# Kernel tuning notes

Hardware: AMD Instinct MI355X
Metric: run time of the kernel (lower is better)

## Reference

```python
import jax, jax.numpy as jnp
import numpy as np

N = 20000; E = 320000; IN = 128; H = 6; C = 64; HC = H * C; NC = 16; NG = 64


def _gatv2(x, src, dst, wl, bl, wr, br, att, bias, heads, out_c, concat):
    # PyG GATv2Conv (eval mode, share_weights=False, negative_slope=0.2)
    n = x.shape[0]
    xl = (x @ wl + bl).reshape(n, heads, out_c)   # source-side transform
    xr = (x @ wr + br).reshape(n, heads, out_c)   # target-side transform
    # edge-wise attention logits: leaky_relu(x_l[j] + x_r[i]) . att
    e = jnp.einsum('ehc,hc->eh', jax.nn.leaky_relu(xl[src] + xr[dst], 0.2), att)
    # segment softmax over incoming edges of each target node
    emax = jax.ops.segment_max(e, dst, num_segments=n)
    a = jnp.exp(e - emax[dst])
    denom = jax.ops.segment_sum(a, dst, num_segments=n)
    alpha = a / (denom[dst] + 1e-16)
    out = jax.ops.segment_sum(xl[src] * alpha[:, :, None], dst, num_segments=n)
    out = out.reshape(n, heads * out_c) if concat else out.mean(axis=1)
    return out + bias


def setup_inputs() -> dict:
    key = jax.random.key(0)
    ks = jax.random.split(key, 32)
    s = 0.05
    inp = {}
    inp['x'] = jax.random.normal(ks[0], (N, IN), jnp.float32)
    inp['edge_index'] = jax.random.randint(ks[1], (2, E), 0, N, dtype=jnp.int32)
    inp['batch'] = jnp.sort(jax.random.randint(ks[2], (N,), 0, NG, dtype=jnp.int32))
    # input projection (input_dim != hidden_dim * n_heads)
    inp['inp_w'] = jax.random.normal(ks[3], (IN, HC), jnp.float32) * s
    inp['inp_b'] = jnp.zeros((HC,), jnp.float32)
    # layer 0: IN -> (H, C), concat
    inp['l0_wl'] = jax.random.normal(ks[4], (IN, HC), jnp.float32) * s
    inp['l0_bl'] = jnp.zeros((HC,), jnp.float32)
    inp['l0_wr'] = jax.random.normal(ks[5], (IN, HC), jnp.float32) * s
    inp['l0_br'] = jnp.zeros((HC,), jnp.float32)
    inp['l0_att'] = jax.random.normal(ks[6], (H, C), jnp.float32) * s
    inp['l0_bias'] = jnp.zeros((HC,), jnp.float32)
    # layer 1: HC -> (H, C), concat
    inp['l1_wl'] = jax.random.normal(ks[7], (HC, HC), jnp.float32) * s
    inp['l1_bl'] = jnp.zeros((HC,), jnp.float32)
    inp['l1_wr'] = jax.random.normal(ks[8], (HC, HC), jnp.float32) * s
    inp['l1_br'] = jnp.zeros((HC,), jnp.float32)
    inp['l1_att'] = jax.random.normal(ks[9], (H, C), jnp.float32) * s
    inp['l1_bias'] = jnp.zeros((HC,), jnp.float32)
    # layer 2: HC -> (1, C), no concat (mean over the single head)
    inp['l2_wl'] = jax.random.normal(ks[10], (HC, C), jnp.float32) * s
    inp['l2_bl'] = jnp.zeros((C,), jnp.float32)
    inp['l2_wr'] = jax.random.normal(ks[11], (HC, C), jnp.float32) * s
    inp['l2_br'] = jnp.zeros((C,), jnp.float32)
    inp['l2_att'] = jax.random.normal(ks[12], (1, C), jnp.float32) * s
    inp['l2_bias'] = jnp.zeros((C,), jnp.float32)
    # residual projection HC -> C at the last layer (bias-free Linear)
    inp['res_w'] = jax.random.normal(ks[13], (HC, C), jnp.float32) * s
    # dense head: Linear(C,C) + BatchNorm1d(eval) + ReLU + Linear(C,NC)
    inp['d1_w'] = jax.random.normal(ks[14], (C, C), jnp.float32) * s
    inp['d1_b'] = jnp.zeros((C,), jnp.float32)
    inp['bn_g'] = jnp.ones((C,), jnp.float32)
    inp['bn_b'] = jnp.zeros((C,), jnp.float32)
    inp['bn_m'] = jnp.zeros((C,), jnp.float32)
    inp['bn_v'] = jnp.ones((C,), jnp.float32)
    inp['d2_w'] = jax.random.normal(ks[15], (C, NC), jnp.float32) * s
    inp['d2_b'] = jnp.zeros((NC,), jnp.float32)
    return inp


def reference(x, edge_index, batch, inp_w, inp_b,
              l0_wl, l0_bl, l0_wr, l0_br, l0_att, l0_bias,
              l1_wl, l1_bl, l1_wr, l1_br, l1_att, l1_bias,
              l2_wl, l2_bl, l2_wr, l2_br, l2_att, l2_bias,
              res_w, d1_w, d1_b, bn_g, bn_b, bn_m, bn_v, d2_w, d2_b):
    n = x.shape[0]
    sl = jnp.arange(n, dtype=edge_index.dtype)           # self-loops (PyG default)
    src = jnp.concatenate([edge_index[0], sl])
    dst = jnp.concatenate([edge_index[1], sl])
    x_res = x @ inp_w + inp_b
    h = jax.nn.elu(_gatv2(x, src, dst, l0_wl, l0_bl, l0_wr, l0_br, l0_att, l0_bias, H, C, True)) + x_res
    x_res = h
    h = jax.nn.elu(_gatv2(h, src, dst, l1_wl, l1_bl, l1_wr, l1_br, l1_att, l1_bias, H, C, True)) + x_res
    x_res = h
    h = jax.nn.elu(_gatv2(h, src, dst, l2_wl, l2_bl, l2_wr, l2_br, l2_att, l2_bias, 1, C, False)) + x_res @ res_w
    pooled = jax.ops.segment_sum(h, batch, num_segments=NG)
    z = pooled @ d1_w + d1_b
    z = (z - bn_m) / jnp.sqrt(bn_v + 1e-5) * bn_g + bn_b  # BatchNorm1d eval
    z = jax.nn.relu(z) @ d2_w + d2_b
    return h, z
```

## Files before the change

kernel.cpp:

```cpp
#include <hip/hip_runtime.h>
#include <hip/hip_bf16.h>
#include <math.h>

#define NN 20000
#define EE 320000
#define IND 128
#define HH 6
#define CC 64
#define HCC 384
#define NCC 16
#define NGG 64

typedef __bf16 bf16x8 __attribute__((ext_vector_type(8)));
typedef float f32x4 __attribute__((ext_vector_type(4)));
typedef float f32x2 __attribute__((ext_vector_type(2)));
typedef unsigned short ushort_t;
typedef unsigned int uint_t;

#define LOG2E 1.44269504088896f

__device__ inline ushort_t f2bf(float f) {
    union { float f; uint_t u; } x; x.f = f;
    uint_t r = (x.u + 0x7FFF + ((x.u >> 16) & 1)) >> 16;
    return (ushort_t)r;
}
__device__ inline void bf8cvt2(uint4 v, f32x2* f) {
    union { uint_t u; float x; } a, b;
    a.u = v.x << 16; b.u = v.x & 0xFFFF0000u; f[0] = (f32x2){a.x, b.x};
    a.u = v.y << 16; b.u = v.y & 0xFFFF0000u; f[1] = (f32x2){a.x, b.x};
    a.u = v.z << 16; b.u = v.z & 0xFFFF0000u; f[2] = (f32x2){a.x, b.x};
    a.u = v.w << 16; b.u = v.w & 0xFFFF0000u; f[3] = (f32x2){a.x, b.x};
}

template <int CTRL>
__device__ inline float dppadd(float x) {
    int y = __builtin_amdgcn_mov_dpp(__builtin_bit_cast(int, x), CTRL, 0xF, 0xF, true);
    return x + __builtin_bit_cast(float, y);
}

__device__ inline void load_lds16(const ushort_t* g, ushort_t* l) {
    __builtin_amdgcn_global_load_lds(
        (const __attribute__((address_space(1))) void*)g,
        (__attribute__((address_space(3))) void*)l, 16, 0, 0);
}


__global__ void zero_init_kernel(int* counts, int* s6_tail, int* s1_tail, int n) {
    int t = blockIdx.x * blockDim.x + threadIdx.x;
    if (t < n) counts[t] = 0;
    if (t < 8) { s6_tail[t] = 0; s1_tail[t] = 0; }
}

__global__ void count_kernel(const int* __restrict__ ei, int* __restrict__ counts, int E) {
    int t = blockIdx.x * blockDim.x + threadIdx.x;
    if (t < E) atomicAdd(&counts[ei[E + t]], 1);
}

__global__ __launch_bounds__(1024) void scan_kernel(
    const int* __restrict__ counts, int* __restrict__ offsets,
    int* __restrict__ cursor, int n) {
    __shared__ int buf[NN];
    __shared__ int part[1024];
    int t = threadIdx.x;
    for (int idx = t; idx < n; idx += 1024) buf[idx] = counts[idx] + 1;
    __syncthreads();
    int per = (n + 1023) / 1024;
    int base = t * per;
    int sum = 0;
    for (int j = 0; j < per; ++j) {
        int idx = base + j;
        if (idx < n) sum += buf[idx];
    }
    part[t] = sum;
    __syncthreads();
    for (int off = 1; off < 1024; off <<= 1) {
        int v = (t >= off) ? part[t - off] : 0;
        __syncthreads();
        part[t] += v;
        __syncthreads();
    }
    int run = (t == 0) ? 0 : part[t - 1];
    for (int j = 0; j < per; ++j) {
        int idx = base + j;
        if (idx < n) {
            int deg = buf[idx];
            buf[idx] = run;
            run += deg;
        }
    }
    __syncthreads();
    for (int idx = t; idx < n; idx += 1024) {
        int v = buf[idx];
        offsets[idx] = v;
        cursor[idx] = v;
    }
    if (t == 1023) offsets[n] = run;
}

__global__ void fill_kernel(const int* __restrict__ ei, int* __restrict__ cursor,
                            int* __restrict__ srcs6, int* __restrict__ srcs1,
                            int E, int n) {
    int t = blockIdx.x * blockDim.x + threadIdx.x;
    if (t < E) {
        int s = ei[t];
        int d = ei[E + t];
        int slot = atomicAdd(&cursor[d], 1);
        srcs6[slot] = s * 1536;
        srcs1[slot] = s << 8;
    } else if (t < E + n) {
        int i = t - E;
        int slot = atomicAdd(&cursor[i], 1);
        srcs6[slot] = i * 1536;
        srcs1[slot] = i << 8;
    }
}

#define WBIG (1152 * IND)
#define WC1 (768 * HCC)
#define WC2 (192 * HCC)
#define XB_N (NN * IND)
#define PREP_TOTAL (WBIG + WC1 + WC2 + XB_N + 1152 + 768 + 192)

__global__ void prep_kernel(const float* __restrict__ x, const float* __restrict__ inp_w,
    const float* __restrict__ l0wl, const float* __restrict__ l0wr,
    const float* __restrict__ l1wl, const float* __restrict__ l1wr,
    const float* __restrict__ l2wl, const float* __restrict__ l2wr,
    const float* __restrict__ resw,
    const float* __restrict__ inp_b,
    const float* __restrict__ l0bl, const float* __restrict__ l0br,
    const float* __restrict__ l1bl, const float* __restrict__ l1br,
    const float* __restrict__ l2bl, const float* __restrict__ l2br,
    ushort_t* wBig, ushort_t* wC1, ushort_t* wC2, ushort_t* xb,
    float* bBig, float* bC1, float* bC2)
{
    int i = blockIdx.x * blockDim.x + threadIdx.x;
    if (i >= PREP_TOTAL) return;
    if (i < WBIG) {
        int col = i >> 7, k = i & 127;
        float v;
        if (col < 384)      v = inp_w[k * 384 + col];
        else if (col < 768) v = l0wl[k * 384 + (col - 384)];
        else                v = l0wr[k * 384 + (col - 768)];
        wBig[i] = f2bf(v); return;
    }
    i -= WBIG;
    if (i < WC1) {
        int col = i / 384, k = i - col * 384;
        float v = col < 384 ? l1wl[k * 384 + col] : l1wr[k * 384 + (col - 384)];
        wC1[i] = f2bf(v); return;
    }
    i -= WC1;
    if (i < WC2) {
        int col = i / 384, k = i - col * 384;
        float v;
        if (col < 64)       v = resw[k * 64 + col];
        else if (col < 128) v = l2wl[k * 64 + (col - 64)];
        else                v = l2wr[k * 64 + (col - 128)];
        wC2[i] = f2bf(v); return;
    }
    i -= WC2;
    if (i < XB_N) { xb[i] = f2bf(x[i]); return; }
    i -= XB_N;
    if (i < 1152) {
        float v;
        if (i < 384)      v = inp_b[i];
        else if (i < 768) v = l0bl[i - 384];
        else              v = l0br[i - 768];
        bBig[i] = v; return;
    }
    i -= 1152;
    if (i < 768) { bC1[i] = i < 384 ? l1bl[i] : l1br[i - 384]; return; }
    i -= 768;
    if (i < 192) {
        float v;
        if (i < 64)       v = 0.0f;
        else if (i < 128) v = l2bl[i - 64];
        else              v = l2br[i - 128];
        bC2[i] = v; return;
    }
}

__global__ __launch_bounds__(512) void gemm_mfma2(
    const ushort_t* __restrict__ A, const ushort_t* __restrict__ BT,
    const float* __restrict__ bias,
    ushort_t* __restrict__ Cb1, int ld1,
    ushort_t* __restrict__ Cb2, int ld2, int split,
    int M, int N, int K, int NT)
{
    __shared__ ushort_t Bs[2][2][128 * 32];
    int t = threadIdx.x;
    int w = t >> 6, L = t & 63;
    int m0 = blockIdx.x * 256;
    int q = L >> 4, r16 = L & 15;
    int lr = L >> 2;
    int lc = ((L & 3) ^ ((lr >> 1) & 3)) * 8;
    int sw = (q ^ ((r16 >> 1) & 3)) * 8;
    int oB = (w * 16) * 32;

    int rA0 = min(m0 + w * 32 + r16, M - 1);
    int rA1 = min(m0 + w * 32 + 16 + r16, M - 1);
    const ushort_t* pA0base = A + (size_t)rA0 * K + q * 8;
    const ushort_t* pA1base = A + (size_t)rA1 * K + q * 8;

    for (int nt = 0; nt < NT; ++nt) {
        int n0 = (blockIdx.y * NT + nt) * 128;
        int rB = min(n0 + w * 16 + lr, N - 1);
        const ushort_t* gB = BT + (size_t)rB * K + lc;
        const ushort_t* pA0 = pA0base;
        const ushort_t* pA1 = pA1base;

        f32x4 acc[2][8];
#pragma unroll
        for (int a = 0; a < 2; ++a)
#pragma unroll
            for (int b = 0; b < 8; ++b) acc[a][b] = (f32x4){0.f, 0.f, 0.f, 0.f};

        load_lds16(gB, &Bs[0][0][oB]);
        load_lds16(gB + 32, &Bs[0][1][oB]);
        gB += 64;
        bf16x8 a0 = *(const bf16x8*)pA0;
        bf16x8 a2 = *(const bf16x8*)(pA0 + 32);
        bf16x8 a1 = *(const bf16x8*)pA1;
        bf16x8 a3 = *(const bf16x8*)(pA1 + 32);
        pA0 += 64; pA1 += 64;

        int buf = 0;
        for (int k0 = 0; k0 < K; k0 += 64) {
            __syncthreads();
            bool more = (k0 + 64 < K);
            if (more) {
                int nb = buf ^ 1;
                load_lds16(gB, &Bs[nb][0][oB]);
                load_lds16(gB + 32, &Bs[nb][1][oB]);
                gB += 64;
            }
            bf16x8 na0, na1, na2, na3;
            if (more) {
                na0 = *(const bf16x8*)pA0;
                na2 = *(const bf16x8*)(pA0 + 32);
                na1 = *(const bf16x8*)pA1;
                na3 = *(const bf16x8*)(pA1 + 32);
                pA0 += 64; pA1 += 64;
            }
#pragma unroll
            for (int ct = 0; ct < 8; ++ct) {
                bf16x8 blo = *(const bf16x8*)&Bs[buf][0][(ct * 16 + r16) * 32 + sw];
                bf16x8 bhi = *(const bf16x8*)&Bs[buf][1][(ct * 16 + r16) * 32 + sw];
                acc[0][ct] = __builtin_amdgcn_mfma_f32_16x16x32_bf16(blo, a0, acc[0][ct], 0, 0, 0);
                acc[1][ct] = __builtin_amdgcn_mfma_f32_16x16x32_bf16(blo, a1, acc[1][ct], 0, 0, 0);
                acc[0][ct] = __builtin_amdgcn_mfma_f32_16x16x32_bf16(bhi, a2, acc[0][ct], 0, 0, 0);
                acc[1][ct] = __builtin_amdgcn_mfma_f32_16x16x32_bf16(bhi, a3, acc[1][ct], 0, 0, 0);
            }
            if (more) { a0 = na0; a1 = na1; a2 = na2; a3 = na3; }
            buf ^= 1;
        }
#pragma unroll
        for (int rt = 0; rt < 2; ++rt) {
            int row = m0 + w * 32 + rt * 16 + r16;
            if (row >= M) continue;
#pragma unroll
            for (int ct = 0; ct < 8; ++ct) {
                int colb = n0 + ct * 16 + q * 4;
                if (colb >= N) continue;
                float4 bv = *(const float4*)(bias + colb);
                uint2 pk;
                pk.x = (uint_t)f2bf(acc[rt][ct][0] + bv.x) | ((uint_t)f2bf(acc[rt][ct][1] + bv.y) << 16);
                pk.y = (uint_t)f2bf(acc[rt][ct][2] + bv.z) | ((uint_t)f2bf(acc[rt][ct][3] + bv.w) << 16);
                if (colb < split)
                    *(uint2*)(Cb1 + (size_t)row * ld1 + colb) = pk;
                else
                    *(uint2*)(Cb2 + (size_t)row * ld2 + (colb - split)) = pk;
            }
        }
    }
}

__global__ __launch_bounds__(256) void gemm_mfma(
    const ushort_t* __restrict__ A, const ushort_t* __restrict__ BT,
    const float* __restrict__ bias,
    float* __restrict__ Cf, ushort_t* __restrict__ Cb1, int ld1,
    ushort_t* __restrict__ Cb2, int ld2, int split,
    int M, int N, int K)
{
    __shared__ ushort_t Bs[2][2][128 * 32];
    int t = threadIdx.x;
    int w = t >> 6, L = t & 63;
    int m0 = blockIdx.x * 128, n0 = blockIdx.y * 128;
    int q = L >> 4, r16 = L & 15;

    f32x4 acc[2][8];
#pragma unroll
    for (int a = 0; a < 2; ++a)
#pragma unroll
        for (int b = 0; b < 8; ++b) acc[a][b] = (f32x4){0.f, 0.f, 0.f, 0.f};

    int lr = L >> 2;
    int lc = ((L & 3) ^ ((lr >> 1) & 3)) * 8;
    int rB0 = min(n0 + w * 32 + lr, N - 1);
    int rB1 = min(n0 + w * 32 + 16 + lr, N - 1);
    const ushort_t* gB0 = BT + (size_t)rB0 * K + lc;
    const ushort_t* gB1 = BT + (size_t)rB1 * K + lc;
    int oB0 = (w * 32) * 32;
    int oB1 = (w * 32 + 16) * 32;

    int rA0 = min(m0 + w * 32 + r16, M - 1);
    int rA1 = min(m0 + w * 32 + 16 + r16, M - 1);
    const ushort_t* pA0 = A + (size_t)rA0 * K + q * 8;
    const ushort_t* pA1 = A + (size_t)rA1 * K + q * 8;

    int sw = (q ^ ((r16 >> 1) & 3)) * 8;

    load_lds16(gB0, &Bs[0][0][oB0]);
    load_lds16(gB1, &Bs[0][0][oB1]);
    load_lds16(gB0 + 32, &Bs[0][1][oB0]);
    load_lds16(gB1 + 32, &Bs[0][1][oB1]);
    gB0 += 64; gB1 += 64;
    bf16x8 a0 = *(const bf16x8*)pA0;
    bf16x8 a2 = *(const bf16x8*)(pA0 + 32);
    bf16x8 a1 = *(const bf16x8*)pA1;
    bf16x8 a3 = *(const bf16x8*)(pA1 + 32);
    pA0 += 64; pA1 += 64;

    int buf = 0;
    for (int k0 = 0; k0 < K; k0 += 64) {
        __syncthreads();
        bool more = (k0 + 64 < K);
        if (more) {
            int nb = buf ^ 1;
            load_lds16(gB0, &Bs[nb][0][oB0]);
            load_lds16(gB1, &Bs[nb][0][oB1]);
            load_lds16(gB0 + 32, &Bs[nb][1][oB0]);
            load_lds16(gB1 + 32, &Bs[nb][1][oB1]);
            gB0 += 64; gB1 += 64;
        }
        bf16x8 na0, na1, na2, na3;
        if (more) {
            na0 = *(const bf16x8*)pA0;
            na2 = *(const bf16x8*)(pA0 + 32);
            na1 = *(const bf16x8*)pA1;
            na3 = *(const bf16x8*)(pA1 + 32);
            pA0 += 64; pA1 += 64;
        }
#pragma unroll
        for (int ct = 0; ct < 8; ++ct) {
            bf16x8 blo = *(const bf16x8*)&Bs[buf][0][(ct * 16 + r16) * 32 + sw];
            bf16x8 bhi = *(const bf16x8*)&Bs[buf][1][(ct * 16 + r16) * 32 + sw];
            acc[0][ct] = __builtin_amdgcn_mfma_f32_16x16x32_bf16(blo, a0, acc[0][ct], 0, 0, 0);
            acc[1][ct] = __builtin_amdgcn_mfma_f32_16x16x32_bf16(blo, a1, acc[1][ct], 0, 0, 0);
            acc[0][ct] = __builtin_amdgcn_mfma_f32_16x16x32_bf16(bhi, a2, acc[0][ct], 0, 0, 0);
            acc[1][ct] = __builtin_amdgcn_mfma_f32_16x16x32_bf16(bhi, a3, acc[1][ct], 0, 0, 0);
        }
        if (more) { a0 = na0; a1 = na1; a2 = na2; a3 = na3; }
        buf ^= 1;
    }
#pragma unroll
    for (int rt = 0; rt < 2; ++rt) {
        int row = m0 + w * 32 + rt * 16 + r16;
        if (row >= M) continue;
#pragma unroll
        for (int ct = 0; ct < 8; ++ct) {
            int colb = n0 + ct * 16 + q * 4;
            if (colb >= N) continue;
            float4 bv = *(const float4*)(bias + colb);
            float v0 = acc[rt][ct][0] + bv.x;
            float v1 = acc[rt][ct][1] + bv.y;
            float v2 = acc[rt][ct][2] + bv.z;
            float v3 = acc[rt][ct][3] + bv.w;
            if (colb < split) {
                if (Cf) {
                    *(float4*)(Cf + (size_t)row * ld1 + colb) = make_float4(v0, v1, v2, v3);
                } else {
                    uint2 pk;
                    pk.x = (uint_t)f2bf(v0) | ((uint_t)f2bf(v1) << 16);
                    pk.y = (uint_t)f2bf(v2) | ((uint_t)f2bf(v3) << 16);
                    *(uint2*)(Cb1 + (size_t)row * ld1 + colb) = pk;
                }
            } else {
                uint2 pk;
                pk.x = (uint_t)f2bf(v0) | ((uint_t)f2bf(v1) << 16);
                pk.y = (uint_t)f2bf(v2) | ((uint_t)f2bf(v3) << 16);
                *(uint2*)(Cb2 + (size_t)row * ld2 + (colb - split)) = pk;
            }
        }
    }
}

__global__ __launch_bounds__(128) void gat6_kernel(
    const ushort_t* __restrict__ cat, const float* __restrict__ att,
    const float* __restrict__ bias, const ushort_t* __restrict__ resB,
    ushort_t* __restrict__ outB,
    const int* __restrict__ offsets, const int* __restrict__ srcs6, int n)
{
    int wid = (blockIdx.x * blockDim.x + threadIdx.x) >> 6;
    if (wid >= n) return;
    int lane = threadIdx.x & 63;
    int h = lane >> 3, c8 = lane & 7;
    bool hv = h < HH;
    int off = h * 64 + c8 * 8;
    int offL2 = (hv ? off : off - 384) * 2;
    int i = wid;
    int beg = __builtin_amdgcn_readfirstlane(offsets[i]);
    int end = __builtin_amdgcn_readfirstlane(offsets[i + 1]);
    int deg = end - beg;
    int P = (deg + 1) >> 1;
    const char* catc = (const char*)cat;

    f32x2 xr2[4], att2[4];
    {
        uint4 v = *(const uint4*)(catc + (size_t)i * 1536 + 768 + offL2);
        bf8cvt2(v, xr2);
    }
#pragma unroll
    for (int j = 0; j < 4; ++j) {
        int o = (offL2 >> 1) + 2 * j;
        att2[j] = (f32x2){att[o] * LOG2E, att[o + 1] * LOG2E};
    }

    float s = 0.0f;
    f32x2 acc2[4];
#pragma unroll
    for (int j = 0; j < 4; ++j) acc2[j] = (f32x2){0.f, 0.f};

    int bA0 = srcs6[beg], bB0 = srcs6[beg + 1];
    uint4 cA = *(const uint4*)(catc + (size_t)(uint_t)bA0 + offL2);
    uint4 cB = *(const uint4*)(catc + (size_t)(uint_t)bB0 + offL2);
    int iA1 = srcs6[beg + 2], iB1 = srcs6[beg + 3];

    for (int p = 0; p < P; ++p) {
        uint4 nA = cA, nB = cB;
        bool pre = (p + 1 < P);
        if (pre) {
            nA = *(const uint4*)(catc + (size_t)(uint_t)iA1 + offL2);
            nB = *(const uint4*)(catc + (size_t)(uint_t)iB1 + offL2);
            iA1 = srcs6[beg + 2 * p + 4];
            iB1 = srcs6[beg + 2 * p + 5];
        }
        f32x2 xlA[4], xlB[4];
        bf8cvt2(cA, xlA);
        bf8cvt2(cB, xlB);
        f32x2 pA2 = (f32x2){0.f, 0.f}, pB2 = (f32x2){0.f, 0.f};
#pragma unroll
        for (int j = 0; j < 4; ++j) {
            f32x2 ta = xlA[j] + xr2[j];
            ta = __builtin_elementwise_max(ta, ta * 0.2f);
            pA2 += ta * att2[j];
            f32x2 tb = xlB[j] + xr2[j];
            tb = __builtin_elementwise_max(tb, tb * 0.2f);
            pB2 += tb * att2[j];
        }
        float pA = pA2.x + pA2.y, pB = pB2.x + pB2.y;
        pA = dppadd<0xB1>(pA);
        pB = dppadd<0xB1>(pB);
        pA = dppadd<0x4E>(pA);
        pB = dppadd<0x4E>(pB);
        pA = dppadd<0x141>(pA);
        pB = dppadd<0x141>(pB);
        float wA = __builtin_amdgcn_exp2f(pA);
        float wB = (2 * p + 1 < deg) ? __builtin_amdgcn_exp2f(pB) : 0.0f;
        s += wA + wB;
        f32x2 wA2 = (f32x2){wA, wA}, wB2 = (f32x2){wB, wB};
#pragma unroll
        for (int j = 0; j < 4; ++j) {
            acc2[j] += wA2 * xlA[j];
            acc2[j] += wB2 * xlB[j];
        }
        cA = nA; cB = nB;
    }

    if (hv) {
        float inv = 1.0f / (s + 1e-16f);
        size_t ob = (size_t)i * HCC + off;
        uint4 rv = *(const uint4*)(resB + ob);
        f32x2 rr[4];
        bf8cvt2(rv, rr);
        ushort_t u[8];
#pragma unroll
        for (int j = 0; j < 4; ++j) {
            float v0 = acc2[j].x * inv + bias[off + 2 * j];
            float v1 = acc2[j].y * inv + bias[off + 2 * j + 1];
            v0 = v0 > 0.0f ? v0 : expm1f(v0);
            v1 = v1 > 0.0f ? v1 : expm1f(v1);
            u[2 * j]     = f2bf(v0 + rr[j].x);
            u[2 * j + 1] = f2bf(v1 + rr[j].y);
        }
        *(uint4*)(outB + ob) = *(uint4*)u;
    }
}

__global__ __launch_bounds__(128) void gat1_kernel(
    const ushort_t* __restrict__ cat, const float* __restrict__ att,
    const float* __restrict__ bias, const float* __restrict__ res,
    float* __restrict__ out,
    const int* __restrict__ offsets, const int* __restrict__ srcs1, int n)
{
    int wid = (blockIdx.x * blockDim.x + threadIdx.x) >> 6;
    if (wid >= n) return;
    int lane = threadIdx.x & 63;
    int e8 = lane >> 3, c8 = lane & 7;
    int i = wid;
    int beg = __builtin_amdgcn_readfirstlane(offsets[i]);
    int end = __builtin_amdgcn_readfirstlane(offsets[i + 1]);
    const char* catc = (const char*)cat;

    f32x2 xr2[4], att2[4];
    {
        uint4 v = *(const uint4*)(cat + (size_t)i * 128 + 64 + c8 * 8);
        bf8cvt2(v, xr2);
    }
#pragma unroll
    for (int j = 0; j < 4; ++j)
        att2[j] = (f32x2){att[c8 * 8 + 2 * j] * LOG2E, att[c8 * 8 + 2 * j + 1] * LOG2E};

    float s = 0.0f;
    f32x2 acc2[4];
#pragma unroll
    for (int j = 0; j < 4; ++j) acc2[j] = (f32x2){0.f, 0.f};

    const uint4 z = make_uint4(0u, 0u, 0u, 0u);
    int p = beg + e8;
    bool val = p < end;
    int b = val ? srcs1[p] : (i << 8);
    uint4 v = *(const uint4*)(catc + (size_t)(uint_t)b + c8 * 16);

    for (int p0 = beg; p0 < end; p0 += 8) {
        uint4 nv = z;
        bool nval = false;
        if (p0 + 8 < end) {
            int np = p0 + 8 + e8;
            nval = np < end;
            int nb = nval ? srcs1[np] : (i << 8);
            nv = *(const uint4*)(catc + (size_t)(uint_t)nb + c8 * 16);
        }
        f32x2 xl[4];
        bf8cvt2(v, xl);
        f32x2 pp2 = (f32x2){0.f, 0.f};
#pragma unroll
        for (int j = 0; j < 4; ++j) {
            f32x2 tv = xl[j] + xr2[j];
            tv = __builtin_elementwise_max(tv, tv * 0.2f);
            pp2 += tv * att2[j];
        }
        float partial = pp2.x + pp2.y;
        partial = dppadd<0xB1>(partial);
        partial = dppadd<0x4E>(partial);
        partial = dppadd<0x141>(partial);
        float wE = val ? __builtin_amdgcn_exp2f(partial) : 0.0f;
        s += wE;
        f32x2 w2 = (f32x2){wE, wE};
#pragma unroll
        for (int j = 0; j < 4; ++j) acc2[j] += w2 * xl[j];
        v = nv;
        val = nval;
    }

    s = dppadd<0x140>(s);
    s += __shfl_xor(s, 16, 64);
    s += __shfl_xor(s, 32, 64);
#pragma unroll
    for (int j = 0; j < 4; ++j) {
        acc2[j].x += __shfl_xor(acc2[j].x, 8, 64);
        acc2[j].y += __shfl_xor(acc2[j].y, 8, 64);
        acc2[j].x += __shfl_xor(acc2[j].x, 16, 64);
        acc2[j].y += __shfl_xor(acc2[j].y, 16, 64);
        acc2[j].x += __shfl_xor(acc2[j].x, 32, 64);
        acc2[j].y += __shfl_xor(acc2[j].y, 32, 64);
    }
    if (e8 == 0) {
        float inv = 1.0f / (s + 1e-16f);
        size_t ob = (size_t)i * CC + c8 * 8;
        float4 r0 = *(const float4*)(res + ob);
        float4 r1 = *(const float4*)(res + ob + 4);
        float rr[8] = {r0.x, r0.y, r0.z, r0.w, r1.x, r1.y, r1.z, r1.w};
        float av[8] = {acc2[0].x, acc2[0].y, acc2[1].x, acc2[1].y,
                       acc2[2].x, acc2[2].y, acc2[3].x, acc2[3].y};
#pragma unroll
        for (int j = 0; j < 8; ++j) {
            float v2 = av[j] * inv + bias[c8 * 8 + j];
            v2 = v2 > 0.0f ? v2 : expm1f(v2);
            av[j] = v2 + rr[j];
        }
        *(float4*)(out + ob) = make_float4(av[0], av[1], av[2], av[3]);
        *(float4*)(out + ob + 4) = make_float4(av[4], av[5], av[6], av[7]);
    }
}

__global__ __launch_bounds__(256) void pool_kernel(const float* __restrict__ h,
                                                   const int* __restrict__ batch,
                                                   float* __restrict__ pooled, int n) {
    int g = blockIdx.x;
    int t = threadIdx.x;
    int w = t >> 6, lane = t & 63;
    int lo = 0, hi = n;
    while (lo < hi) { int mid = (lo + hi) >> 1; if (batch[mid] < g) lo = mid + 1; else hi = mid; }
    int start = lo;
    int hi2 = n;
    while (lo < hi2) { int mid = (lo + hi2) >> 1; if (batch[mid] < g + 1) lo = mid + 1; else hi2 = mid; }
    int endd = lo;
    float acc = 0.0f;
    for (int r = start + w; r < endd; r += 4)
        acc += h[(size_t)r * 64 + lane];
    __shared__ float red[4][64];
    red[w][lane] = acc;
    __syncthreads();
    if (w == 0)
        pooled[g * 64 + lane] = red[0][lane] + red[1][lane] + red[2][lane] + red[3][lane];
}

__global__ void head_kernel(const float* __restrict__ pooled,
                            const float* __restrict__ d1w, const float* __restrict__ d1b,
                            const float* __restrict__ bng, const float* __restrict__ bnb,
                            const float* __restrict__ bnm, const float* __restrict__ bnv,
                            const float* __restrict__ d2w, const float* __restrict__ d2b,
                            float* __restrict__ zout) {
    __shared__ float z1[64 * 64];
    int t = threadIdx.x;
    for (int idx = t; idx < 64 * 64; idx += 256) {
        int r = idx >> 6, c = idx & 63;
        float acc = d1b[c];
        for (int k = 0; k < 64; ++k) acc += pooled[r * 64 + k] * d1w[k * 64 + c];
        acc = (acc - bnm[c]) / sqrtf(bnv[c] + 1e-5f) * bng[c] + bnb[c];
        z1[idx] = acc > 0.0f ? acc : 0.0f;
    }
    __syncthreads();
    for (int idx = t; idx < 64 * NCC; idx += 256) {
        int r = idx >> 4, c = idx & 15;
        float acc = d2b[c];
        for (int k = 0; k < 64; ++k) acc += z1[r * 64 + k] * d2w[k * NCC + c];
        zout[idx] = acc;
    }
}


extern "C" void kernel_launch(void* const* d_in, const int* in_sizes, int n_in,
                              void* d_out, int out_size, void* d_ws, size_t ws_size,
                              hipStream_t stream) {
    const int N = NN, E = EE, C = CC, HC = HCC, NG = NGG;
    const int EN = E + N;

    const float* x     = (const float*)d_in[0];
    const int*   ei    = (const int*)d_in[1];
    const int*   batch = (const int*)d_in[2];
    const float* inp_w = (const float*)d_in[3];
    const float* inp_b = (const float*)d_in[4];
    const float* l0_wl = (const float*)d_in[5];
    const float* l0_bl = (const float*)d_in[6];
    const float* l0_wr = (const float*)d_in[7];
    const float* l0_br = (const float*)d_in[8];
    const float* l0_att = (const float*)d_in[9];
    const float* l0_bias = (const float*)d_in[10];
    const float* l1_wl = (const float*)d_in[11];
    const float* l1_bl = (const float*)d_in[12];
    const float* l1_wr = (const float*)d_in[13];
    const float* l1_br = (const float*)d_in[14];
    const float* l1_att = (const float*)d_in[15];
    const float* l1_bias = (const float*)d_in[16];
    const float* l2_wl = (const float*)d_in[17];
    const float* l2_bl = (const float*)d_in[18];
    const float* l2_wr = (const float*)d_in[19];
    const float* l2_br = (const float*)d_in[20];
    const float* l2_att = (const float*)d_in[21];
    const float* l2_bias = (const float*)d_in[22];
    const float* res_w = (const float*)d_in[23];
    const float* d1_w = (const float*)d_in[24];
    const float* d1_b = (const float*)d_in[25];
    const float* bn_g = (const float*)d_in[26];
    const float* bn_b = (const float*)d_in[27];
    const float* bn_m = (const float*)d_in[28];
    const float* bn_v = (const float*)d_in[29];
    const float* d2_w = (const float*)d_in[30];
    const float* d2_b = (const float*)d_in[31];

    float* out = (float*)d_out;

    char* ws = (char*)d_ws;
    size_t off = 0;
    auto alloc = [&](size_t bytes) -> void* {
        void* p = ws + off;
        off += (bytes + 255) & ~(size_t)255;
        return p;
    };
    ushort_t* bufH_b  = (ushort_t*)alloc((size_t)N * HC * 2);
    ushort_t* cat01_b = (ushort_t*)alloc((size_t)N * 768 * 2 + 2048);
    ushort_t* xres_b  = (ushort_t*)alloc((size_t)N * HC * 2);
    ushort_t* cat2_b  = (ushort_t*)alloc((size_t)N * 128 * 2);
    float*    bufRes  = (float*)alloc((size_t)N * C * 4);
    ushort_t* xb      = (ushort_t*)alloc((size_t)N * IND * 2);
    ushort_t* wBig    = (ushort_t*)alloc((size_t)WBIG * 2);
    ushort_t* wC1     = (ushort_t*)alloc((size_t)WC1 * 2);
    ushort_t* wC2     = (ushort_t*)alloc((size_t)WC2 * 2);
    float*    bBig    = (float*)alloc((size_t)1152 * 4);
    float*    bC1     = (float*)alloc((size_t)768 * 4);
    float*    bC2     = (float*)alloc((size_t)192 * 4);
    int*      counts  = (int*)alloc((size_t)N * 4);
    int*      cursor  = (int*)alloc((size_t)N * 4);
    int*      offsets = (int*)alloc((size_t)(N + 1) * 4);
    int*      srcs6   = (int*)alloc((size_t)(EN + 8) * 4);
    int*      srcs1   = (int*)alloc((size_t)(EN + 8) * 4);
    float*    pooled  = (float*)alloc((size_t)NG * C * 4);

    zero_init_kernel<<<(N + 255) / 256, 256, 0, stream>>>(counts, srcs6 + EN, srcs1 + EN, N);
    count_kernel<<<(E + 255) / 256, 256, 0, stream>>>(ei, counts, E);
    scan_kernel<<<1, 1024, 0, stream>>>(counts, offsets, cursor, N);
    fill_kernel<<<(EN + 255) / 256, 256, 0, stream>>>(ei, cursor, srcs6, srcs1, E, N);
    prep_kernel<<<(PREP_TOTAL + 255) / 256, 256, 0, stream>>>(
        x, inp_w, l0_wl, l0_wr, l1_wl, l1_wr, l2_wl, l2_wr, res_w,
        inp_b, l0_bl, l0_br, l1_bl, l1_br, l2_bl, l2_br,
        wBig, wC1, wC2, xb, bBig, bC1, bC2);

    int mtiles256 = (N + 255) / 256;
    int mtiles = (N + 127) / 128;
    dim3 gblk(128);
    int gatBlocks = (N * 64 + 127) / 128;

    gemm_mfma2<<<dim3(mtiles256, 3), dim3(512), 0, stream>>>(xb, wBig, bBig,
        xres_b, HC, cat01_b, 768, 384, N, 1152, IND, 3);
    gat6_kernel<<<gatBlocks, gblk, 0, stream>>>(cat01_b, l0_att, l0_bias,
                                                xres_b, bufH_b, offsets, srcs6, N);
    gemm_mfma2<<<dim3(mtiles256, 3), dim3(512), 0, stream>>>(bufH_b, wC1, bC1,
        nullptr, 0, cat01_b, 768, 0, N, 768, HC, 2);
    gat6_kernel<<<gatBlocks, gblk, 0, stream>>>(cat01_b, l1_att, l1_bias,
                                                bufH_b, bufH_b, offsets, srcs6, N);
    gemm_mfma<<<dim3(mtiles, 2), dim3(256), 0, stream>>>(bufH_b, wC2, bC2,
        bufRes, nullptr, C, cat2_b, 128, 64, N, 192, HC);
    gat1_kernel<<<gatBlocks, gblk, 0, stream>>>(cat2_b, l2_att, l2_bias,
                                                bufRes, out, offsets, srcs1, N);
    pool_kernel<<<NG, 256, 0, stream>>>(out, batch, pooled, N);
    head_kernel<<<1, 256, 0, stream>>>(pooled, d1_w, d1_b, bn_g, bn_b, bn_m, bn_v,
                                       d2_w, d2_b, out + (size_t)N * C);
}
```

Before: 428.6 us.

## Swizzle GEMM blocks across XCDs, split pooling into quarters, stage head weights in LDS

Remaps GEMM workgroup indices so that consecutive logical tiles land on the same XCD, aiming for better L2 reuse of shared A/B tiles. The pool kernel now launches four blocks per graph, each summing a quarter of the rows and combining through float atomics into a buffer zeroed at init. The head kernel first copies pooled values and dense weights into shared memory. Atomics make the pooled sum order nondeterministic, and the swizzle only pays off if the workgroup-to-XCD dispatch order matches the assumed round-robin.

```diff
diff --git a/kernel.cpp b/kernel.cpp
--- a/kernel.cpp
+++ b/kernel.cpp
@@ -44,10 +44,18 @@
         (__attribute__((address_space(3))) void*)l, 16, 0, 0);
 }
 
-
-__global__ void zero_init_kernel(int* counts, int* s6_tail, int* s1_tail, int n) {
+__device__ inline int xcd_swz(int lin, int nwg) {
+    int q = nwg >> 3, r = nwg & 7;
+    int xc = lin & 7, j = lin >> 3;
+    return (xc < r ? xc * (q + 1) : r * (q + 1) + (xc - r) * q) + j;
+}
+
+
+__global__ void zero_init_kernel(int* counts, int* s6_tail, int* s1_tail,
+                                 float* pooled, int n, int np) {
     int t = blockIdx.x * blockDim.x + threadIdx.x;
     if (t < n) counts[t] = 0;
+    if (t < np) pooled[t] = 0.0f;
     if (t < 8) { s6_tail[t] = 0; s1_tail[t] = 0; }
 }
 
@@ -190,7 +198,11 @@
     __shared__ ushort_t Bs[2][2][128 * 32];
     int t = threadIdx.x;
     int w = t >> 6, L = t & 63;
-    int m0 = blockIdx.x * 256;
+    int nwg = gridDim.x * gridDim.y;
+    int logical = xcd_swz(blockIdx.y * gridDim.x + blockIdx.x, nwg);
+    int bx = logical % gridDim.x;
+    int by = logical / gridDim.x;
+    int m0 = bx * 256;
     int q = L >> 4, r16 = L & 15;
     int lr = L >> 2;
     int lc = ((L & 3) ^ ((lr >> 1) & 3)) * 8;
@@ -203,7 +215,7 @@
     const ushort_t* pA1base = A + (size_t)rA1 * K + q * 8;
 
     for (int nt = 0; nt < NT; ++nt) {
-        int n0 = (blockIdx.y * NT + nt) * 128;
+        int n0 = (by * NT + nt) * 128;
         int rB = min(n0 + w * 16 + lr, N - 1);
         const ushort_t* gB = BT + (size_t)rB * K + lc;
         const ushort_t* pA0 = pA0base;
@@ -285,7 +297,10 @@
     __shared__ ushort_t Bs[2][2][128 * 32];
     int t = threadIdx.x;
     int w = t >> 6, L = t & 63;
-    int m0 = blockIdx.x * 128, n0 = blockIdx.y * 128;
+    int nwg = gridDim.x * gridDim.y;
+    int logical = xcd_swz(blockIdx.y * gridDim.x + blockIdx.x, nwg);
+    int m0 = (logical % gridDim.x) * 128;
+    int n0 = (logical / gridDim.x) * 128;
     int q = L >> 4, r16 = L & 15;
 
     f32x4 acc[2][8];
@@ -587,7 +602,8 @@
 __global__ __launch_bounds__(256) void pool_kernel(const float* __restrict__ h,
                                                    const int* __restrict__ batch,
                                                    float* __restrict__ pooled, int n) {
-    int g = blockIdx.x;
+    int b = blockIdx.x;
+    int g = b >> 2, qd = b & 3;
     int t = threadIdx.x;
     int w = t >> 6, lane = t & 63;
     int lo = 0, hi = n;
@@ -596,28 +612,43 @@
     int hi2 = n;
     while (lo < hi2) { int mid = (lo + hi2) >> 1; if (batch[mid] < g + 1) lo = mid + 1; else hi2 = mid; }
     int endd = lo;
+    int len = endd - start;
+    int q0 = start + (len * qd) / 4;
+    int q1 = start + (len * (qd + 1)) / 4;
     float acc = 0.0f;
-    for (int r = start + w; r < endd; r += 4)
+    for (int r = q0 + w; r < q1; r += 4)
         acc += h[(size_t)r * 64 + lane];
     __shared__ float red[4][64];
     red[w][lane] = acc;
     __syncthreads();
-    if (w == 0)
-        pooled[g * 64 + lane] = red[0][lane] + red[1][lane] + red[2][lane] + red[3][lane];
-}
-
-__global__ void head_kernel(const float* __restrict__ pooled,
+    if (w == 0) {
+        float v2 = red[0][lane] + red[1][lane] + red[2][lane] + red[3][lane];
+        atomicAdd(&pooled[g * 64 + lane], v2);
+    }
+}
+
+__global__ __launch_bounds__(256) void head_kernel(const float* __restrict__ pooled,
                             const float* __restrict__ d1w, const float* __restrict__ d1b,
                             const float* __restrict__ bng, const float* __restrict__ bnb,
                             const float* __restrict__ bnm, const float* __restrict__ bnv,
                             const float* __restrict__ d2w, const float* __restrict__ d2b,
                             float* __restrict__ zout) {
+    __shared__ float pl[64 * 64];
+    __shared__ float w1[64 * 64];
+    __shared__ float w2[64 * NCC];
     __shared__ float z1[64 * 64];
     int t = threadIdx.x;
+    for (int i = t * 4; i < 64 * 64; i += 1024) {
+        *(float4*)&pl[i] = *(const float4*)&pooled[i];
+        *(float4*)&w1[i] = *(const float4*)&d1w[i];
+    }
+    for (int i = t * 4; i < 64 * NCC; i += 1024)
+        *(float4*)&w2[i] = *(const float4*)&d2w[i];
+    __syncthreads();
     for (int idx = t; idx < 64 * 64; idx += 256) {
         int r = idx >> 6, c = idx & 63;
         float acc = d1b[c];
-        for (int k = 0; k < 64; ++k) acc += pooled[r * 64 + k] * d1w[k * 64 + c];
+        for (int k = 0; k < 64; ++k) acc += pl[r * 64 + k] * w1[k * 64 + c];
         acc = (acc - bnm[c]) / sqrtf(bnv[c] + 1e-5f) * bng[c] + bnb[c];
         z1[idx] = acc > 0.0f ? acc : 0.0f;
     }
@@ -625,7 +656,7 @@
     for (int idx = t; idx < 64 * NCC; idx += 256) {
         int r = idx >> 4, c = idx & 15;
         float acc = d2b[c];
-        for (int k = 0; k < 64; ++k) acc += z1[r * 64 + k] * d2w[k * NCC + c];
+        for (int k = 0; k < 64; ++k) acc += z1[r * 64 + k] * w2[k * NCC + c];
         zout[idx] = acc;
     }
 }
@@ -698,7 +729,8 @@
     int*      srcs1   = (int*)alloc((size_t)(EN + 8) * 4);
     float*    pooled  = (float*)alloc((size_t)NG * C * 4);
 
-    zero_init_kernel<<<(N + 255) / 256, 256, 0, stream>>>(counts, srcs6 + EN, srcs1 + EN, N);
+    zero_init_kernel<<<(N + 255) / 256, 256, 0, stream>>>(counts, srcs6 + EN, srcs1 + EN,
+                                                          pooled, N, NG * C);
     count_kernel<<<(E + 255) / 256, 256, 0, stream>>>(ei, counts, E);
     scan_kernel<<<1, 1024, 0, stream>>>(counts, offsets, cursor, N);
     fill_kernel<<<(EN + 255) / 256, 256, 0, stream>>>(ei, cursor, srcs6, srcs1, E, N);
@@ -724,7 +756,7 @@
         bufRes, nullptr, C, cat2_b, 128, 64, N, 192, HC);
     gat1_kernel<<<gatBlocks, gblk, 0, stream>>>(cat2_b, l2_att, l2_bias,
                                                 bufRes, out, offsets, srcs1, N);
-    pool_kernel<<<NG, 256, 0, stream>>>(out, batch, pooled, N);
+    pool_kernel<<<NG * 4, 256, 0, stream>>>(out, batch, pooled, N);
     head_kernel<<<1, 256, 0, stream>>>(pooled, d1_w, d1_b, bn_g, bn_b, bn_m, bn_v,
                                        d2_w, d2_b, out + (size_t)N * C);
 }
```

Result: faster. 402.6 us (-6.1%).
